# Kernel optimization log

Hardware: AMD Instinct MI355X
Metric: run time of the kernel (lower is better)

## Reference

```python
import jax, jax.numpy as jnp
import numpy as np

B, T, D = 2, 2048, 1024
N, H = 16, 64  # num_heads, head_dim


def setup_inputs() -> dict:
    key = jax.random.key(0)
    ks = jax.random.split(key, 8)
    glorot = lambda k, shape, fan_in, fan_out: jax.random.uniform(
        k, shape, jnp.float32, -1.0, 1.0) * np.sqrt(6.0 / (fan_in + fan_out))
    return {
        "q": jax.random.normal(ks[0], (B, T, D), jnp.float32),
        "v": jax.random.normal(ks[1], (B, T, D), jnp.float32),
        "k": jax.random.normal(ks[2], (B, T, D), jnp.float32),
        "w_query": glorot(ks[3], (D, N, H), D, N * H),
        "b_query": jnp.zeros((N, 1, H), jnp.float32),
        "w_value": glorot(ks[4], (D, N, H), D, N * H),
        "b_value": jnp.zeros((N, 1, H), jnp.float32),
        "w_key": glorot(ks[5], (D, N, H), D, N * H),
        "b_key": jnp.zeros((N, 1, H), jnp.float32),
        "w_projection": glorot(ks[6], (N, D, H), N * H, D),
        "b_projection": jnp.zeros((1, D), jnp.float32),
    }


def reference(q, v, k, w_query, b_query, w_value, b_value, w_key, b_key,
              w_projection, b_projection):
    # QKV projections: [B,T,D] x [D,N,H] -> [B,N,T,H]
    query = jnp.einsum('btd,dnh->bnth', q, w_query) + b_query
    value = jnp.einsum('btd,dnh->bnth', v, w_value) + b_value
    key_p = jnp.einsum('btd,dnh->bnth', k, w_key) + b_key
    # Scaled dot-product attention, scores divided by sqrt(head_dim)
    scale = 1.0 / jnp.sqrt(jnp.asarray(H, query.dtype))
    scores = jnp.einsum('bnth,bnsh->bnts', query, key_p) * scale  # [B,N,T,T]
    weights = jax.nn.softmax(scores, axis=-1)
    attn = jnp.einsum('bnts,bnsh->bnth', weights, value)
    # Output projection: [B,N,T,H] x [N,D,H] -> [B,T,D]
    out = jnp.einsum('bnth,ndh->btd', attn, w_projection) + b_projection
    return out
```

## Files before the change

### kernel.cpp

```cpp
#include <hip/hip_runtime.h>
#include <hip/hip_bf16.h>
#include <cstdint>
#include <cstddef>


typedef __attribute__((ext_vector_type(8))) short short8;
typedef __attribute__((ext_vector_type(4))) short short4v;
typedef __attribute__((ext_vector_type(4))) float floatx4;
typedef __attribute__((ext_vector_type(8))) unsigned short ushort8;

#define EXP2F(x) __builtin_amdgcn_exp2f(x)

#if defined(__has_builtin)
#if __has_builtin(__builtin_amdgcn_mfma_f32_16x16x16bf16_1k)
#define HAVE_MFMA16 1
#endif
#endif

static __device__ __forceinline__ unsigned short f2bf(float f) {
    union { float f; unsigned int u; } v; v.f = f;
    unsigned int r = v.u + 0x7fffu + ((v.u >> 16) & 1u);
    return (unsigned short)(r >> 16);
}
static __device__ __forceinline__ unsigned int pk2bf(float lo, float hi) {
    __hip_bfloat162 t = __float22bfloat162_rn(make_float2(lo, hi));
    union { __hip_bfloat162 h; unsigned int u; } c; c.h = t;
    return c.u;
}
static __device__ __forceinline__ void gl_lds16(const unsigned short* g, unsigned short* l) {
    __builtin_amdgcn_global_load_lds(
        (const __attribute__((address_space(1))) unsigned int*)g,
        (__attribute__((address_space(3))) unsigned int*)l, 16, 0, 0);
}

__global__ __launch_bounds__(256) void mha_transpose_w(
    const float* __restrict__ wq, const float* __restrict__ wk, const float* __restrict__ wv,
    unsigned short* __restrict__ wqT, unsigned short* __restrict__ wkT, unsigned short* __restrict__ wvT)
{
    __shared__ float tile[32][33];
    const float* src; unsigned short* dst;
    int z = blockIdx.z;
    if (z == 0)      { src = wq; dst = wqT; }
    else if (z == 1) { src = wk; dst = wkT; }
    else             { src = wv; dst = wvT; }
    int n0 = blockIdx.x * 32, d0 = blockIdx.y * 32;
    int tx = threadIdx.x, ty = threadIdx.y;
    #pragma unroll
    for (int j = 0; j < 4; ++j)
        tile[ty + j * 8][tx] = src[(size_t)(d0 + ty + j * 8) * 1024 + n0 + tx];
    __syncthreads();
    #pragma unroll
    for (int j = 0; j < 4; ++j)
        dst[(size_t)(n0 + ty + j * 8) * 1024 + d0 + tx] = f2bf(tile[tx][ty + j * 8]);
}

__global__ __launch_bounds__(256) void mha_reorder_wp(
    const float* __restrict__ wp, unsigned short* __restrict__ wp2)
{
    int base = blockIdx.x * 1024 + threadIdx.x;
    #pragma unroll
    for (int i = 0; i < 4; ++i) {
        int idx = base + i * 256;
        int n = idx >> 16, d = (idx >> 6) & 1023, h = idx & 63;
        wp2[(size_t)d * 1024 + n * 64 + h] = f2bf(wp[idx]);
    }
}

__global__ __launch_bounds__(256) void prep_bf16_3(
    const float* __restrict__ x0, const float* __restrict__ x1, const float* __restrict__ x2,
    unsigned short* __restrict__ o0, unsigned short* __restrict__ o1, unsigned short* __restrict__ o2)
{
    int y = blockIdx.y;
    const float* x = y == 0 ? x0 : (y == 1 ? x1 : x2);
    unsigned short* o = y == 0 ? o0 : (y == 1 ? o1 : o2);
    size_t i = ((size_t)blockIdx.x * 256 + threadIdx.x) * 8;
    float4 a = *(const float4*)(x + i);
    float4 b = *(const float4*)(x + i + 4);
    uint4 pk;
    pk.x = pk2bf(a.x, a.y); pk.y = pk2bf(a.z, a.w);
    pk.z = pk2bf(b.x, b.y); pk.w = pk2bf(b.z, b.w);
    *(uint4*)(o + i) = pk;
}

__global__ __launch_bounds__(256) void gemm_qkv128(
    const unsigned short* __restrict__ A0, const unsigned short* __restrict__ A1,
    const unsigned short* __restrict__ A2,
    const unsigned short* __restrict__ W0, const unsigned short* __restrict__ W1,
    const unsigned short* __restrict__ W2,
    const float* __restrict__ b0, const float* __restrict__ b1, const float* __restrict__ b2,
    unsigned short* __restrict__ O0, unsigned short* __restrict__ O1, unsigned short* __restrict__ O2,
    float qscale, int matSel)
{
    __shared__ unsigned short As[128 * 32];
    __shared__ unsigned short Bs[128 * 32];
    int bm = blockIdx.x, by = blockIdx.y;
    int mat, nt;
    if (matSel < 0) { mat = by >> 3; nt = by & 7; } else { mat = matSel; nt = by; }
    const unsigned short* A  = mat == 0 ? A0 : (mat == 1 ? A1 : A2);
    const unsigned short* WT = mat == 0 ? W0 : (mat == 1 ? W1 : W2);
    const float* bias        = mat == 0 ? b0 : (mat == 1 ? b1 : b2);
    unsigned short* Out      = mat == 0 ? O0 : (mat == 1 ? O1 : O2);
    float scale = (mat == 0) ? qscale : 1.0f;
    int vmode = (mat == 2);

    int tid = threadIdx.x;
    int w = tid >> 6, lane = tid & 63, c15 = lane & 15, quad = lane >> 4;
    int wm = w >> 1, wn = w & 1;

    const unsigned short* gA[2]; unsigned short* lA[2];
    const unsigned short* gB[2]; unsigned short* lB[2];
    #pragma unroll
    for (int i = 0; i < 2; ++i) {
        int s = (w * 2 + i) * 64 + lane;
        gA[i] = A  + (size_t)(bm * 128 + (s >> 2)) * 1024 + (s & 3) * 8;
        lA[i] = &As[s * 8];
        gB[i] = WT + (size_t)(nt * 128 + (s >> 2)) * 1024 + (s & 3) * 8;
        lB[i] = &Bs[s * 8];
    }

    floatx4 acc[4][4];
    #pragma unroll
    for (int mi = 0; mi < 4; ++mi)
        #pragma unroll
        for (int ni = 0; ni < 4; ++ni) acc[mi][ni] = (floatx4){0.f, 0.f, 0.f, 0.f};

    for (int kt = 0; kt < 32; ++kt) {
        __syncthreads();
        #pragma unroll
        for (int i = 0; i < 2; ++i) { gl_lds16(gA[i] + kt * 32, lA[i]); gl_lds16(gB[i] + kt * 32, lB[i]); }
        __syncthreads();
        short8 af[4], bfr[4];
        #pragma unroll
        for (int mi = 0; mi < 4; ++mi)
            af[mi] = *(const short8*)&As[(wm * 64 + mi * 16 + c15) * 32 + quad * 8];
        #pragma unroll
        for (int ni = 0; ni < 4; ++ni)
            bfr[ni] = *(const short8*)&Bs[(wn * 64 + ni * 16 + c15) * 32 + quad * 8];
        #pragma unroll
        for (int mi = 0; mi < 4; ++mi)
            #pragma unroll
            for (int ni = 0; ni < 4; ++ni)
                acc[mi][ni] = __builtin_amdgcn_mfma_f32_16x16x32_bf16(af[mi], bfr[ni], acc[mi][ni], 0, 0, 0);
    }
    #pragma unroll
    for (int mi = 0; mi < 4; ++mi)
        #pragma unroll
        for (int ni = 0; ni < 4; ++ni)
            #pragma unroll
            for (int r = 0; r < 4; ++r) {
                int row = bm * 128 + wm * 64 + mi * 16 + quad * 4 + r;
                int col = nt * 128 + wn * 64 + ni * 16 + c15;
                float val = (acc[mi][ni][r] + bias[col]) * scale;
                int b = row >> 11, t = row & 2047, n = col >> 6, h = col & 63;
                if (vmode)
                    Out[((size_t)(b * 16 + n) * 64 + h) * 2048 + t] = f2bf(val);
                else
                    Out[((size_t)(b * 16 + n) * 2048 + t) * 64 + h] = f2bf(val);
            }
}

__global__ __launch_bounds__(256) void mha_flash4(
    const unsigned short* __restrict__ Qp, const unsigned short* __restrict__ Kp,
    const unsigned short* __restrict__ Vt, unsigned short* __restrict__ attnb)
{
    __shared__ unsigned short Ks[64 * 72];
    __shared__ unsigned short Vs[64 * 72];
#ifndef HAVE_MFMA16
    __shared__ unsigned short Pl[4][32 * 72];
#endif

    int bi = blockIdx.x;
    int xcd = bi & 7, jj = bi >> 3;
    int bn = xcd * 4 + (jj >> 4), qt = jj & 15;
    int b = bn >> 4, n = bn & 15;
    int tid = threadIdx.x;
    int w = tid >> 6, lane = tid & 63, c15 = lane & 15, quad = lane >> 4;

    const unsigned short* Qb = Qp + (size_t)bn * 2048 * 64;
    const unsigned short* Kb = Kp + (size_t)bn * 2048 * 64;
    const unsigned short* Vb = Vt + (size_t)bn * 64 * 2048;

    int qbase = qt * 128 + w * 32;

    short8 bQ[2][2];
    #pragma unroll
    for (int tni = 0; tni < 2; ++tni)
        #pragma unroll
        for (int kc = 0; kc < 2; ++kc)
            bQ[tni][kc] = *(const short8*)(Qb + (size_t)(qbase + tni * 16 + c15) * 64 + kc * 32 + quad * 8);

    float l_i[2] = {0.f, 0.f};
    floatx4 oT[4][2];
    #pragma unroll
    for (int i = 0; i < 4; ++i)
        #pragma unroll
        for (int j2 = 0; j2 < 2; ++j2) oT[i][j2] = (floatx4){0.f, 0.f, 0.f, 0.f};

    int srow = tid >> 3, scc = tid & 7;

    ushort8 kreg[2], vreg[2];
    #pragma unroll
    for (int i = 0; i < 2; ++i) {
        kreg[i] = *(const ushort8*)(Kb + (size_t)(srow + i * 32) * 64 + scc * 8);
        vreg[i] = *(const ushort8*)(Vb + (size_t)(srow + i * 32) * 2048 + scc * 8);
    }

    for (int it = 0; it < 32; ++it) {
        __syncthreads();
        #pragma unroll
        for (int i = 0; i < 2; ++i) {
            *(ushort8*)&Ks[(srow + i * 32) * 72 + scc * 8] = kreg[i];
            *(ushort8*)&Vs[(srow + i * 32) * 72 + scc * 8] = vreg[i];
        }
        if (it < 31) {
            int s1 = (it + 1) * 64;
            #pragma unroll
            for (int i = 0; i < 2; ++i) {
                kreg[i] = *(const ushort8*)(Kb + (size_t)(s1 + srow + i * 32) * 64 + scc * 8);
                vreg[i] = *(const ushort8*)(Vb + (size_t)(srow + i * 32) * 2048 + s1 + scc * 8);
            }
        }
        __syncthreads();

        floatx4 sc[4][2];
        #pragma unroll
        for (int smi = 0; smi < 4; ++smi) {
            short8 a0 = *(const short8*)&Ks[(smi * 16 + c15) * 72 + quad * 8];
            short8 a1 = *(const short8*)&Ks[(smi * 16 + c15) * 72 + 32 + quad * 8];
            #pragma unroll
            for (int tni = 0; tni < 2; ++tni) {
                floatx4 t = (floatx4){0.f, 0.f, 0.f, 0.f};
                t = __builtin_amdgcn_mfma_f32_16x16x32_bf16(a0, bQ[tni][0], t, 0, 0, 0);
                t = __builtin_amdgcn_mfma_f32_16x16x32_bf16(a1, bQ[tni][1], t, 0, 0, 0);
                sc[smi][tni] = t;
            }
        }
#ifdef HAVE_MFMA16
        short4v pB[4][2];
#endif
        #pragma unroll
        for (int tni = 0; tni < 2; ++tni) {
            float rs = 0.f;
            #pragma unroll
            for (int smi = 0; smi < 4; ++smi) {
                float p0 = EXP2F(sc[smi][tni][0]);
                float p1 = EXP2F(sc[smi][tni][1]);
                float p2 = EXP2F(sc[smi][tni][2]);
                float p3 = EXP2F(sc[smi][tni][3]);
                rs += (p0 + p1) + (p2 + p3);
                uint2 pw;
                pw.x = pk2bf(p0, p1);
                pw.y = pk2bf(p2, p3);
#ifdef HAVE_MFMA16
                union { uint2 u; short4v s; } cv; cv.u = pw;
                pB[smi][tni] = cv.s;
#else
                *(uint2*)&Pl[w][(tni * 16 + c15) * 72 + smi * 16 + quad * 4] = pw;
#endif
            }
            l_i[tni] += rs;
        }
#ifdef HAVE_MFMA16
        #pragma unroll
        for (int hmi = 0; hmi < 4; ++hmi)
            #pragma unroll
            for (int smi = 0; smi < 4; ++smi) {
                short4v aV = *(const short4v*)&Vs[(hmi * 16 + c15) * 72 + smi * 16 + quad * 4];
                #pragma unroll
                for (int tni = 0; tni < 2; ++tni)
                    oT[hmi][tni] = __builtin_amdgcn_mfma_f32_16x16x16bf16_1k(
                        aV, pB[smi][tni], oT[hmi][tni], 0, 0, 0);
            }
#else
        #pragma unroll
        for (int sk = 0; sk < 2; ++sk) {
            short8 bP[2];
            #pragma unroll
            for (int tni = 0; tni < 2; ++tni)
                bP[tni] = *(const short8*)&Pl[w][(tni * 16 + c15) * 72 + sk * 32 + quad * 8];
            #pragma unroll
            for (int hmi = 0; hmi < 4; ++hmi) {
                short8 aV = *(const short8*)&Vs[(hmi * 16 + c15) * 72 + sk * 32 + quad * 8];
                #pragma unroll
                for (int tni = 0; tni < 2; ++tni)
                    oT[hmi][tni] = __builtin_amdgcn_mfma_f32_16x16x32_bf16(aV, bP[tni], oT[hmi][tni], 0, 0, 0);
            }
        }
#endif
    }
    float lf[2];
    #pragma unroll
    for (int tni = 0; tni < 2; ++tni) {
        float s = l_i[tni];
        s += __shfl_xor(s, 16, 64);
        s += __shfl_xor(s, 32, 64);
        lf[tni] = 1.0f / s;
    }
    #pragma unroll
    for (int hmi = 0; hmi < 4; ++hmi)
        #pragma unroll
        for (int tni = 0; tni < 2; ++tni) {
            int t = qbase + tni * 16 + c15;
            uint2 ow;
            ow.x = pk2bf(oT[hmi][tni][0] * lf[tni], oT[hmi][tni][1] * lf[tni]);
            ow.y = pk2bf(oT[hmi][tni][2] * lf[tni], oT[hmi][tni][3] * lf[tni]);
            *(uint2*)&attnb[(size_t)(b * 2048 + t) * 1024 + n * 64 + hmi * 16 + quad * 4] = ow;
        }
}

__global__ __launch_bounds__(256) void gemm_out64v2(
    const unsigned short* __restrict__ A, const unsigned short* __restrict__ BT,
    const float* __restrict__ bias, float* __restrict__ out)
{
    __shared__ unsigned short As[64 * 64];
    __shared__ unsigned short Bs[128 * 64];
    int bm = blockIdx.x, nt = blockIdx.y;
    int tid = threadIdx.x;
    int w = tid >> 6, lane = tid & 63, c15 = lane & 15, quad = lane >> 4;
    int wm = w >> 1, wn = w & 1;

    const unsigned short* gA[2]; unsigned short* lA[2];
    const unsigned short* gB[4]; unsigned short* lB[4];
    #pragma unroll
    for (int i = 0; i < 2; ++i) {
        int s = (w * 2 + i) * 64 + lane;
        int row = s >> 3, cl = (s & 7) ^ (row & 7);
        gA[i] = A + (size_t)(bm * 64 + row) * 1024 + cl * 8;
        lA[i] = &As[s * 8];
    }
    #pragma unroll
    for (int i = 0; i < 4; ++i) {
        int s = (w * 4 + i) * 64 + lane;
        int row = s >> 3, cl = (s & 7) ^ (row & 7);
        gB[i] = BT + (size_t)(nt * 128 + row) * 1024 + cl * 8;
        lB[i] = &Bs[s * 8];
    }

    floatx4 acc[2][4];
    #pragma unroll
    for (int mi = 0; mi < 2; ++mi)
        #pragma unroll
        for (int ni = 0; ni < 4; ++ni) acc[mi][ni] = (floatx4){0.f, 0.f, 0.f, 0.f};

    for (int kt = 0; kt < 16; ++kt) {
        __syncthreads();
        #pragma unroll
        for (int i = 0; i < 2; ++i) gl_lds16(gA[i] + kt * 64, lA[i]);
        #pragma unroll
        for (int i = 0; i < 4; ++i) gl_lds16(gB[i] + kt * 64, lB[i]);
        __syncthreads();
        #pragma unroll
        for (int kc = 0; kc < 2; ++kc) {
            short8 af[2], bfr[4];
            #pragma unroll
            for (int mi = 0; mi < 2; ++mi) {
                int row = wm * 32 + mi * 16 + c15;
                af[mi] = *(const short8*)&As[row * 64 + (((kc * 4 + quad) ^ (row & 7)) * 8)];
            }
            #pragma unroll
            for (int ni = 0; ni < 4; ++ni) {
                int row = wn * 64 + ni * 16 + c15;
                bfr[ni] = *(const short8*)&Bs[row * 64 + (((kc * 4 + quad) ^ (row & 7)) * 8)];
            }
            #pragma unroll
            for (int mi = 0; mi < 2; ++mi)
                #pragma unroll
                for (int ni = 0; ni < 4; ++ni)
                    acc[mi][ni] = __builtin_amdgcn_mfma_f32_16x16x32_bf16(af[mi], bfr[ni], acc[mi][ni], 0, 0, 0);
        }
    }
    #pragma unroll
    for (int mi = 0; mi < 2; ++mi)
        #pragma unroll
        for (int ni = 0; ni < 4; ++ni)
            #pragma unroll
            for (int r = 0; r < 4; ++r) {
                int row = bm * 64 + wm * 32 + mi * 16 + quad * 4 + r;
                int col = nt * 128 + wn * 64 + ni * 16 + c15;
                out[(size_t)row * 1024 + col] = acc[mi][ni][r] + bias[col];
            }
}

extern "C" void kernel_launch(void* const* d_in, const int* in_sizes, int n_in,
                              void* d_out, int out_size, void* d_ws, size_t ws_size,
                              hipStream_t stream)
{
    const float* q  = (const float*)d_in[0];
    const float* v  = (const float*)d_in[1];
    const float* k  = (const float*)d_in[2];
    const float* wq = (const float*)d_in[3];
    const float* bq = (const float*)d_in[4];
    const float* wv = (const float*)d_in[5];
    const float* bv = (const float*)d_in[6];
    const float* wk = (const float*)d_in[7];
    const float* bk = (const float*)d_in[8];
    const float* wp = (const float*)d_in[9];
    const float* bp = (const float*)d_in[10];
    float* out = (float*)d_out;

    char* ws = (char*)d_ws;
    unsigned short* wqT  = (unsigned short*)(ws + (size_t)0);
    unsigned short* wkT  = (unsigned short*)(ws + ((size_t)2  << 20));
    unsigned short* wvT  = (unsigned short*)(ws + ((size_t)4  << 20));
    unsigned short* wp2  = (unsigned short*)(ws + ((size_t)6  << 20));
    unsigned short* Qp   = (unsigned short*)(ws + ((size_t)8  << 20));
    unsigned short* Kp   = (unsigned short*)(ws + ((size_t)16 << 20));
    unsigned short* Vtp  = (unsigned short*)(ws + ((size_t)24 << 20));
    unsigned short* Xb   = (unsigned short*)(ws + ((size_t)32 << 20));
    unsigned short* attnb= (unsigned short*)(ws + ((size_t)32 << 20));

    const float qscale = 0.125f * 1.44269504088896f;

    hipLaunchKernelGGL(mha_transpose_w, dim3(32, 32, 3), dim3(32, 8), 0, stream,
                       wq, wk, wv, wqT, wkT, wvT);
    hipLaunchKernelGGL(mha_reorder_wp, dim3(1024), dim3(256), 0, stream, wp, wp2);

    if (ws_size >= ((size_t)64 << 20)) {
        unsigned short* qb = (unsigned short*)(ws + ((size_t)40 << 20));
        unsigned short* kb = (unsigned short*)(ws + ((size_t)48 << 20));
        unsigned short* vb = (unsigned short*)(ws + ((size_t)56 << 20));
        hipLaunchKernelGGL(prep_bf16_3, dim3(2048, 3), dim3(256), 0, stream, q, k, v, qb, kb, vb);
        hipLaunchKernelGGL(gemm_qkv128, dim3(32, 24), dim3(256), 0, stream,
                           qb, kb, vb, wqT, wkT, wvT, bq, bk, bv, Qp, Kp, Vtp, qscale, -1);
    } else {
        hipLaunchKernelGGL(prep_bf16_3, dim3(2048, 1), dim3(256), 0, stream, q, q, q, Xb, Xb, Xb);
        hipLaunchKernelGGL(gemm_qkv128, dim3(32, 8), dim3(256), 0, stream,
                           Xb, Xb, Xb, wqT, wkT, wvT, bq, bk, bv, Qp, Kp, Vtp, qscale, 0);
        hipLaunchKernelGGL(prep_bf16_3, dim3(2048, 1), dim3(256), 0, stream, k, k, k, Xb, Xb, Xb);
        hipLaunchKernelGGL(gemm_qkv128, dim3(32, 8), dim3(256), 0, stream,
                           Xb, Xb, Xb, wqT, wkT, wvT, bq, bk, bv, Qp, Kp, Vtp, qscale, 1);
        hipLaunchKernelGGL(prep_bf16_3, dim3(2048, 1), dim3(256), 0, stream, v, v, v, Xb, Xb, Xb);
        hipLaunchKernelGGL(gemm_qkv128, dim3(32, 8), dim3(256), 0, stream,
                           Xb, Xb, Xb, wqT, wkT, wvT, bq, bk, bv, Qp, Kp, Vtp, qscale, 2);
    }

    hipLaunchKernelGGL(mha_flash4, dim3(512), dim3(256), 0, stream, Qp, Kp, Vtp, attnb);
    hipLaunchKernelGGL(gemm_out64v2, dim3(64, 8), dim3(256), 0, stream, attnb, wp2, bp, out);
}
```

Before: 231.1 us.

## Fuse prep kernels, widen QKV GEMM K-tile with swizzle, double-buffer flash LDS

Merges the weight transpose, projection-weight reorder and input bf16 conversion into a single launch to cut launch overhead. The QKV GEMM now stages 64-wide K tiles with an XOR-swizzled LDS layout, halving the number of barrier iterations while avoiding bank conflicts. The attention kernel double-buffers K/V in LDS with the same swizzle, dropping one barrier per iteration and overlapping the stores with compute. The cost is more LDS per block, which could reduce occupancy.

```diff
diff --git a/kernel.cpp b/kernel.cpp
--- a/kernel.cpp
+++ b/kernel.cpp
@@ -31,6 +31,55 @@
     __builtin_amdgcn_global_load_lds(
         (const __attribute__((address_space(1))) unsigned int*)g,
         (__attribute__((address_space(3))) unsigned int*)l, 16, 0, 0);
+}
+
+__global__ __launch_bounds__(256) void mha_prep_all(
+    const float* __restrict__ q, const float* __restrict__ k, const float* __restrict__ v,
+    const float* __restrict__ wq, const float* __restrict__ wk, const float* __restrict__ wv,
+    const float* __restrict__ wp,
+    unsigned short* __restrict__ wqT, unsigned short* __restrict__ wkT,
+    unsigned short* __restrict__ wvT, unsigned short* __restrict__ wp2,
+    unsigned short* __restrict__ qb, unsigned short* __restrict__ kb,
+    unsigned short* __restrict__ vb)
+{
+    __shared__ float tile[32][33];
+    int bid = blockIdx.x, tid = threadIdx.x;
+    if (bid < 3072) {
+        int z = bid >> 10, r = bid & 1023;
+        const float* src; unsigned short* dst;
+        if (z == 0)      { src = wq; dst = wqT; }
+        else if (z == 1) { src = wk; dst = wkT; }
+        else             { src = wv; dst = wvT; }
+        int n0 = (r & 31) * 32, d0 = (r >> 5) * 32;
+        int tx = tid & 31, ty = tid >> 5;
+        #pragma unroll
+        for (int j = 0; j < 4; ++j)
+            tile[ty + j * 8][tx] = src[(size_t)(d0 + ty + j * 8) * 1024 + n0 + tx];
+        __syncthreads();
+        #pragma unroll
+        for (int j = 0; j < 4; ++j)
+            dst[(size_t)(n0 + ty + j * 8) * 1024 + d0 + tx] = f2bf(tile[tx][ty + j * 8]);
+    } else if (bid < 4096) {
+        int base = (bid - 3072) * 1024 + tid;
+        #pragma unroll
+        for (int i = 0; i < 4; ++i) {
+            int idx = base + i * 256;
+            int n = idx >> 16, d = (idx >> 6) & 1023, h = idx & 63;
+            wp2[(size_t)d * 1024 + n * 64 + h] = f2bf(wp[idx]);
+        }
+    } else {
+        int j = bid - 4096;
+        int y = j >> 11, x = j & 2047;
+        const float* src = y == 0 ? q : (y == 1 ? k : v);
+        unsigned short* o = y == 0 ? qb : (y == 1 ? kb : vb);
+        size_t i = ((size_t)x * 256 + tid) * 8;
+        float4 a = *(const float4*)(src + i);
+        float4 b2 = *(const float4*)(src + i + 4);
+        uint4 pk;
+        pk.x = pk2bf(a.x, a.y); pk.y = pk2bf(a.z, a.w);
+        pk.z = pk2bf(b2.x, b2.y); pk.w = pk2bf(b2.z, b2.w);
+        *(uint4*)(o + i) = pk;
+    }
 }
 
 __global__ __launch_bounds__(256) void mha_transpose_w(
@@ -53,7 +102,6 @@
     for (int j = 0; j < 4; ++j)
         dst[(size_t)(n0 + ty + j * 8) * 1024 + d0 + tx] = f2bf(tile[tx][ty + j * 8]);
 }
-
 __global__ __launch_bounds__(256) void mha_reorder_wp(
     const float* __restrict__ wp, unsigned short* __restrict__ wp2)
 {
@@ -65,7 +113,6 @@
         wp2[(size_t)d * 1024 + n * 64 + h] = f2bf(wp[idx]);
     }
 }
-
 __global__ __launch_bounds__(256) void prep_bf16_3(
     const float* __restrict__ x0, const float* __restrict__ x1, const float* __restrict__ x2,
     unsigned short* __restrict__ o0, unsigned short* __restrict__ o1, unsigned short* __restrict__ o2)
@@ -82,7 +129,7 @@
     *(uint4*)(o + i) = pk;
 }
 
-__global__ __launch_bounds__(256) void gemm_qkv128(
+__global__ __launch_bounds__(256) void gemm_qkv128v2(
     const unsigned short* __restrict__ A0, const unsigned short* __restrict__ A1,
     const unsigned short* __restrict__ A2,
     const unsigned short* __restrict__ W0, const unsigned short* __restrict__ W1,
@@ -91,8 +138,8 @@
     unsigned short* __restrict__ O0, unsigned short* __restrict__ O1, unsigned short* __restrict__ O2,
     float qscale, int matSel)
 {
-    __shared__ unsigned short As[128 * 32];
-    __shared__ unsigned short Bs[128 * 32];
+    __shared__ unsigned short As[128 * 64];
+    __shared__ unsigned short Bs[128 * 64];
     int bm = blockIdx.x, by = blockIdx.y;
     int mat, nt;
     if (matSel < 0) { mat = by >> 3; nt = by & 7; } else { mat = matSel; nt = by; }
@@ -107,14 +154,15 @@
     int w = tid >> 6, lane = tid & 63, c15 = lane & 15, quad = lane >> 4;
     int wm = w >> 1, wn = w & 1;
 
-    const unsigned short* gA[2]; unsigned short* lA[2];
-    const unsigned short* gB[2]; unsigned short* lB[2];
-    #pragma unroll
-    for (int i = 0; i < 2; ++i) {
-        int s = (w * 2 + i) * 64 + lane;
-        gA[i] = A  + (size_t)(bm * 128 + (s >> 2)) * 1024 + (s & 3) * 8;
+    const unsigned short* gA[4]; unsigned short* lA[4];
+    const unsigned short* gB[4]; unsigned short* lB[4];
+    #pragma unroll
+    for (int i = 0; i < 4; ++i) {
+        int s = (w * 4 + i) * 64 + lane;
+        int row = s >> 3, lc = (s & 7) ^ (row & 7);
+        gA[i] = A  + (size_t)(bm * 128 + row) * 1024 + lc * 8;
         lA[i] = &As[s * 8];
-        gB[i] = WT + (size_t)(nt * 128 + (s >> 2)) * 1024 + (s & 3) * 8;
+        gB[i] = WT + (size_t)(nt * 128 + row) * 1024 + lc * 8;
         lB[i] = &Bs[s * 8];
     }
 
@@ -124,23 +172,31 @@
         #pragma unroll
         for (int ni = 0; ni < 4; ++ni) acc[mi][ni] = (floatx4){0.f, 0.f, 0.f, 0.f};
 
-    for (int kt = 0; kt < 32; ++kt) {
+    int x7 = c15 & 7;
+    for (int kt = 0; kt < 16; ++kt) {
         __syncthreads();
         #pragma unroll
-        for (int i = 0; i < 2; ++i) { gl_lds16(gA[i] + kt * 32, lA[i]); gl_lds16(gB[i] + kt * 32, lB[i]); }
+        for (int i = 0; i < 4; ++i) { gl_lds16(gA[i] + kt * 64, lA[i]); gl_lds16(gB[i] + kt * 64, lB[i]); }
         __syncthreads();
-        short8 af[4], bfr[4];
-        #pragma unroll
-        for (int mi = 0; mi < 4; ++mi)
-            af[mi] = *(const short8*)&As[(wm * 64 + mi * 16 + c15) * 32 + quad * 8];
-        #pragma unroll
-        for (int ni = 0; ni < 4; ++ni)
-            bfr[ni] = *(const short8*)&Bs[(wn * 64 + ni * 16 + c15) * 32 + quad * 8];
-        #pragma unroll
-        for (int mi = 0; mi < 4; ++mi)
-            #pragma unroll
-            for (int ni = 0; ni < 4; ++ni)
-                acc[mi][ni] = __builtin_amdgcn_mfma_f32_16x16x32_bf16(af[mi], bfr[ni], acc[mi][ni], 0, 0, 0);
+        #pragma unroll
+        for (int kc = 0; kc < 2; ++kc) {
+            short8 af[4], bfr[4];
+            #pragma unroll
+            for (int mi = 0; mi < 4; ++mi) {
+                int row = wm * 64 + mi * 16 + c15;
+                af[mi] = *(const short8*)&As[row * 64 + (((kc * 4 + quad) ^ x7) * 8)];
+            }
+            #pragma unroll
+            for (int ni = 0; ni < 4; ++ni) {
+                int row = wn * 64 + ni * 16 + c15;
+                bfr[ni] = *(const short8*)&Bs[row * 64 + (((kc * 4 + quad) ^ x7) * 8)];
+            }
+            #pragma unroll
+            for (int mi = 0; mi < 4; ++mi)
+                #pragma unroll
+                for (int ni = 0; ni < 4; ++ni)
+                    acc[mi][ni] = __builtin_amdgcn_mfma_f32_16x16x32_bf16(af[mi], bfr[ni], acc[mi][ni], 0, 0, 0);
+        }
     }
     #pragma unroll
     for (int mi = 0; mi < 4; ++mi)
@@ -159,12 +215,12 @@
             }
 }
 
-__global__ __launch_bounds__(256) void mha_flash4(
+__global__ __launch_bounds__(256) void mha_flash5(
     const unsigned short* __restrict__ Qp, const unsigned short* __restrict__ Kp,
     const unsigned short* __restrict__ Vt, unsigned short* __restrict__ attnb)
 {
-    __shared__ unsigned short Ks[64 * 72];
-    __shared__ unsigned short Vs[64 * 72];
+    __shared__ unsigned short Ks[2][64 * 64];
+    __shared__ unsigned short Vs[2][64 * 64];
 #ifndef HAVE_MFMA16
     __shared__ unsigned short Pl[4][32 * 72];
 #endif
@@ -175,6 +231,7 @@
     int b = bn >> 4, n = bn & 15;
     int tid = threadIdx.x;
     int w = tid >> 6, lane = tid & 63, c15 = lane & 15, quad = lane >> 4;
+    int x7 = c15 & 7;
 
     const unsigned short* Qb = Qp + (size_t)bn * 2048 * 64;
     const unsigned short* Kb = Kp + (size_t)bn * 2048 * 64;
@@ -197,6 +254,8 @@
         for (int j2 = 0; j2 < 2; ++j2) oT[i][j2] = (floatx4){0.f, 0.f, 0.f, 0.f};
 
     int srow = tid >> 3, scc = tid & 7;
+    int woff0 = srow * 64 + ((scc ^ (srow & 7)) * 8);
+    int woff1 = woff0 + 32 * 64;
 
     ushort8 kreg[2], vreg[2];
     #pragma unroll
@@ -204,14 +263,14 @@
         kreg[i] = *(const ushort8*)(Kb + (size_t)(srow + i * 32) * 64 + scc * 8);
         vreg[i] = *(const ushort8*)(Vb + (size_t)(srow + i * 32) * 2048 + scc * 8);
     }
+    *(ushort8*)&Ks[0][woff0] = kreg[0];
+    *(ushort8*)&Ks[0][woff1] = kreg[1];
+    *(ushort8*)&Vs[0][woff0] = vreg[0];
+    *(ushort8*)&Vs[0][woff1] = vreg[1];
+    __syncthreads();
 
     for (int it = 0; it < 32; ++it) {
-        __syncthreads();
-        #pragma unroll
-        for (int i = 0; i < 2; ++i) {
-            *(ushort8*)&Ks[(srow + i * 32) * 72 + scc * 8] = kreg[i];
-            *(ushort8*)&Vs[(srow + i * 32) * 72 + scc * 8] = vreg[i];
-        }
+        int cur = it & 1;
         if (it < 31) {
             int s1 = (it + 1) * 64;
             #pragma unroll
@@ -220,13 +279,15 @@
                 vreg[i] = *(const ushort8*)(Vb + (size_t)(srow + i * 32) * 2048 + s1 + scc * 8);
             }
         }
-        __syncthreads();
+        const unsigned short* Kc = &Ks[cur][0];
+        const unsigned short* Vc = &Vs[cur][0];
 
         floatx4 sc[4][2];
         #pragma unroll
         for (int smi = 0; smi < 4; ++smi) {
-            short8 a0 = *(const short8*)&Ks[(smi * 16 + c15) * 72 + quad * 8];
-            short8 a1 = *(const short8*)&Ks[(smi * 16 + c15) * 72 + 32 + quad * 8];
+            int rowK = (smi * 16 + c15) * 64;
+            short8 a0 = *(const short8*)&Kc[rowK + ((quad ^ x7) * 8)];
+            short8 a1 = *(const short8*)&Kc[rowK + (((4 + quad) ^ x7) * 8)];
             #pragma unroll
             for (int tni = 0; tni < 2; ++tni) {
                 floatx4 t = (floatx4){0.f, 0.f, 0.f, 0.f};
@@ -262,15 +323,18 @@
         }
 #ifdef HAVE_MFMA16
         #pragma unroll
-        for (int hmi = 0; hmi < 4; ++hmi)
+        for (int hmi = 0; hmi < 4; ++hmi) {
+            int rowV = (hmi * 16 + c15) * 64;
             #pragma unroll
             for (int smi = 0; smi < 4; ++smi) {
-                short4v aV = *(const short4v*)&Vs[(hmi * 16 + c15) * 72 + smi * 16 + quad * 4];
+                int lc = 2 * smi + (quad >> 1);
+                short4v aV = *(const short4v*)&Vc[rowV + ((lc ^ x7) * 8) + (quad & 1) * 4];
                 #pragma unroll
                 for (int tni = 0; tni < 2; ++tni)
                     oT[hmi][tni] = __builtin_amdgcn_mfma_f32_16x16x16bf16_1k(
                         aV, pB[smi][tni], oT[hmi][tni], 0, 0, 0);
             }
+        }
 #else
         #pragma unroll
         for (int sk = 0; sk < 2; ++sk) {
@@ -280,13 +344,21 @@
                 bP[tni] = *(const short8*)&Pl[w][(tni * 16 + c15) * 72 + sk * 32 + quad * 8];
             #pragma unroll
             for (int hmi = 0; hmi < 4; ++hmi) {
-                short8 aV = *(const short8*)&Vs[(hmi * 16 + c15) * 72 + sk * 32 + quad * 8];
+                int rowV = (hmi * 16 + c15) * 64;
+                short8 aV = *(const short8*)&Vc[rowV + (((sk * 4 + quad) ^ x7) * 8)];
                 #pragma unroll
                 for (int tni = 0; tni < 2; ++tni)
                     oT[hmi][tni] = __builtin_amdgcn_mfma_f32_16x16x32_bf16(aV, bP[tni], oT[hmi][tni], 0, 0, 0);
             }
         }
 #endif
+        if (it < 31) {
+            *(ushort8*)&Ks[cur ^ 1][woff0] = kreg[0];
+            *(ushort8*)&Ks[cur ^ 1][woff1] = kreg[1];
+            *(ushort8*)&Vs[cur ^ 1][woff0] = vreg[0];
+            *(ushort8*)&Vs[cur ^ 1][woff1] = vreg[1];
+            __syncthreads();
+        }
     }
     float lf[2];
     #pragma unroll
@@ -411,29 +483,29 @@
 
     const float qscale = 0.125f * 1.44269504088896f;
 
-    hipLaunchKernelGGL(mha_transpose_w, dim3(32, 32, 3), dim3(32, 8), 0, stream,
-                       wq, wk, wv, wqT, wkT, wvT);
-    hipLaunchKernelGGL(mha_reorder_wp, dim3(1024), dim3(256), 0, stream, wp, wp2);
-
     if (ws_size >= ((size_t)64 << 20)) {
         unsigned short* qb = (unsigned short*)(ws + ((size_t)40 << 20));
         unsigned short* kb = (unsigned short*)(ws + ((size_t)48 << 20));
         unsigned short* vb = (unsigned short*)(ws + ((size_t)56 << 20));
-        hipLaunchKernelGGL(prep_bf16_3, dim3(2048, 3), dim3(256), 0, stream, q, k, v, qb, kb, vb);
-        hipLaunchKernelGGL(gemm_qkv128, dim3(32, 24), dim3(256), 0, stream,
+        hipLaunchKernelGGL(mha_prep_all, dim3(10240), dim3(256), 0, stream,
+                           q, k, v, wq, wk, wv, wp, wqT, wkT, wvT, wp2, qb, kb, vb);
+        hipLaunchKernelGGL(gemm_qkv128v2, dim3(32, 24), dim3(256), 0, stream,
                            qb, kb, vb, wqT, wkT, wvT, bq, bk, bv, Qp, Kp, Vtp, qscale, -1);
     } else {
+        hipLaunchKernelGGL(mha_transpose_w, dim3(32, 32, 3), dim3(32, 8), 0, stream,
+                           wq, wk, wv, wqT, wkT, wvT);
+        hipLaunchKernelGGL(mha_reorder_wp, dim3(1024), dim3(256), 0, stream, wp, wp2);
         hipLaunchKernelGGL(prep_bf16_3, dim3(2048, 1), dim3(256), 0, stream, q, q, q, Xb, Xb, Xb);
-        hipLaunchKernelGGL(gemm_qkv128, dim3(32, 8), dim3(256), 0, stream,
+        hipLaunchKernelGGL(gemm_qkv128v2, dim3(32, 8), dim3(256), 0, stream,
                            Xb, Xb, Xb, wqT, wkT, wvT, bq, bk, bv, Qp, Kp, Vtp, qscale, 0);
         hipLaunchKernelGGL(prep_bf16_3, dim3(2048, 1), dim3(256), 0, stream, k, k, k, Xb, Xb, Xb);
-        hipLaunchKernelGGL(gemm_qkv128, dim3(32, 8), dim3(256), 0, stream,
+        hipLaunchKernelGGL(gemm_qkv128v2, dim3(32, 8), dim3(256), 0, stream,
                            Xb, Xb, Xb, wqT, wkT, wvT, bq, bk, bv, Qp, Kp, Vtp, qscale, 1);
         hipLaunchKernelGGL(prep_bf16_3, dim3(2048, 1), dim3(256), 0, stream, v, v, v, Xb, Xb, Xb);
-        hipLaunchKernelGGL(gemm_qkv128, dim3(32, 8), dim3(256), 0, stream,
+        hipLaunchKernelGGL(gemm_qkv128v2, dim3(32, 8), dim3(256), 0, stream,
                            Xb, Xb, Xb, wqT, wkT, wvT, bq, bk, bv, Qp, Kp, Vtp, qscale, 2);
     }
 
-    hipLaunchKernelGGL(mha_flash4, dim3(512), dim3(256), 0, stream, Qp, Kp, Vtp, attnb);
+    hipLaunchKernelGGL(mha_flash5, dim3(512), dim3(256), 0, stream, Qp, Kp, Vtp, attnb);
     hipLaunchKernelGGL(gemm_out64v2, dim3(64, 8), dim3(256), 0, stream, attnb, wp2, bp, out);
 }
```

After: 242.8 us. +5.0%, slower.
